# Kernel optimization log

Measured on AMD Instinct MI355X. Metric: run time of the kernel, lower is better.

## Reference

```python
import jax, jax.numpy as jnp
from jax import lax
import numpy as np

B, T, I, H, O = 256, 1024, 64, 25, 64

def setup_inputs() -> dict:
    key = jax.random.key(0)
    ks = jax.random.split(key, 7)
    s_ih = 1.0 / np.sqrt(H)  # PyTorch LSTM init scale (uniform +-1/sqrt(H))
    return {
        "x": jax.random.normal(ks[0], (B, T, I), dtype=jnp.float32),
        "W_ih": jax.random.uniform(ks[1], (4 * H, I), minval=-s_ih, maxval=s_ih, dtype=jnp.float32),
        "W_hh": jax.random.uniform(ks[2], (4 * H, H), minval=-s_ih, maxval=s_ih, dtype=jnp.float32),
        "b_ih": jax.random.uniform(ks[3], (4 * H,), minval=-s_ih, maxval=s_ih, dtype=jnp.float32),
        "b_hh": jax.random.uniform(ks[4], (4 * H,), minval=-s_ih, maxval=s_ih, dtype=jnp.float32),
        "W_fc": jax.random.uniform(ks[5], (O, H), minval=-s_ih, maxval=s_ih, dtype=jnp.float32),
        "b_fc": jax.random.uniform(ks[6], (O,), minval=-s_ih, maxval=s_ih, dtype=jnp.float32),
    }

def reference(x, W_ih, W_hh, b_ih, b_hh, W_fc, b_fc):
    # x: [B, T, I]; PyTorch LSTM gate order: i, f, g, o
    Bh = x.shape[0]
    Hh = W_hh.shape[1]
    # Precompute the input contribution to all gates for all timesteps (one big GEMM).
    gates_x = jnp.einsum('bti,gi->btg', x, W_ih) + b_ih + b_hh  # [B, T, 4H]

    def step(carry, gx):
        h, c = carry
        g = gx + h @ W_hh.T                     # [B, 4H]
        i, f, gg, o = jnp.split(g, 4, axis=-1)
        i = jax.nn.sigmoid(i)
        f = jax.nn.sigmoid(f)
        gg = jnp.tanh(gg)
        o = jax.nn.sigmoid(o)
        c = f * c + i * gg
        h = o * jnp.tanh(c)
        return (h, c), h

    h0 = jnp.zeros((Bh, Hh), dtype=x.dtype)
    c0 = jnp.zeros((Bh, Hh), dtype=x.dtype)
    _, hs = lax.scan(step, (h0, c0), jnp.swapaxes(gates_x, 0, 1))  # hs: [T, B, H]
    hs = jnp.swapaxes(hs, 0, 1)                                   # [B, T, H]
    return hs @ W_fc.T + b_fc                                     # [B, T, O]
```

## Files before the change

### kernel.cpp

```cpp
#include <hip/hip_runtime.h>
#include <hip/hip_fp16.h>


#define Bn 256
#define Tn 1024
#define In 64
#define Hn 25
#define Gn 100
#define On 64
#define CH 16
#define NCH (Tn / CH)

#define SCL_S -1.44269504089f
#define SCL_T -2.88539008178f

typedef __attribute__((ext_vector_type(8))) short short8;
typedef __attribute__((ext_vector_type(4))) float f32x4;
typedef __attribute__((ext_vector_type(4))) int i32x4;

__device__ __forceinline__ float frcp(float x) { return __builtin_amdgcn_rcpf(x); }
__device__ __forceinline__ float ex2(float x) {
    float r;
    asm("v_exp_f32 %0, %1\n\ts_nop 1" : "=v"(r) : "v"(x));
    return r;
}
__device__ __forceinline__ float bcast(float v, int lane) {
    return __int_as_float(__builtin_amdgcn_readlane(__float_as_int(v), lane));
}
__device__ __forceinline__ float xswap(float x) {
    float a = x, b = x;
    asm("s_nop 0\n\tv_permlane32_swap_b32 %0, %1\n\ts_nop 0"
        : "+v"(a), "+v"(b));
    return b;
}
__device__ __forceinline__ unsigned short f2bf(float f) {
    unsigned u = __float_as_uint(f);
    return (unsigned short)((u + 0x7FFFu + ((u >> 16) & 1u)) >> 16);
}
__device__ __forceinline__ int pk2(float lo, float hi) {
    return (int)(((unsigned)f2bf(hi) << 16) | f2bf(lo));
}

__device__ __forceinline__ void colmap(int n, int& g, float& scl) {
    if (n < 50) {
        const int r = n >> 1;
        g = ((n & 1) ? 2 : 0) * Hn + r;
        scl = (n & 1) ? SCL_T : SCL_S;
    } else {
        const int m = n - 50, r = m >> 1;
        g = ((m & 1) ? 3 : 1) * Hn + r;
        scl = SCL_S;
    }
}

__global__ __launch_bounds__(192, 1)
void lstm_fused(const float* __restrict__ x, const float* __restrict__ W_ih,
                const float* __restrict__ W_hh, const float* __restrict__ b_ih,
                const float* __restrict__ b_hh, const float* __restrict__ W_fc,
                const float* __restrict__ b_fc, float* __restrict__ out) {
    __shared__ short lB[112 * 72];
    __shared__ float lbias[112];
    __shared__ short xlds[16 * 72];
    __shared__ float gbuf[2][CH * 100];
    __shared__ float hbuf[32][64];

    const int tid  = threadIdx.x;
    const int wid  = tid >> 6;
    const int lane = tid & 63;
    const int b    = blockIdx.x;

    for (int i = tid; i < 112 * 64; i += 192) {
        const int n = i >> 6, k = i & 63;
        float v = 0.f;
        if (n < Gn) {
            int g; float scl;
            colmap(n, g, scl);
            v = W_ih[(size_t)g * In + k] * scl;
        }
        lB[n * 72 + k] = (short)f2bf(v);
    }
    if (tid < 112) {
        float v = 0.f;
        if (tid < Gn) {
            int g; float scl;
            colmap(tid, g, scl);
            v = (b_ih[g] + b_hh[g]) * scl;
        }
        lbias[tid] = v;
    }
    __syncthreads();

    float wAv[25], wBv[25];
    float c = 0.f, h = 0.f;
    float sB = 1.f, dB = 0.f;
    int coff = 0;
    float wFC[25];
    float bfc = 0.f;
    float* op = nullptr;
    short8 bf0[7], bf1[7];
    float biasv[7];
    float4 xr0, xr1, xr2, xr3;
    const float* xb = x + (size_t)b * Tn * In;

    const int quad = lane >> 4;
    const int l16  = lane & 15;

    if (wid == 0) {
        const bool lo = lane < 32;
        const int rr  = min(lane & 31, Hn - 1);
        const float sclA = SCL_S;
        const float sclB = lo ? SCL_T : SCL_S;
        sB = lo ? 2.f : 1.f;
        dB = lo ? -1.f : 0.f;
        const float* rowA = W_hh + (size_t)((lo ? 0 : 1) * Hn + rr) * Hn;
        const float* rowB = W_hh + (size_t)((lo ? 2 : 3) * Hn + rr) * Hn;
#pragma unroll
        for (int j = 0; j < 25; ++j) {
            wAv[j] = rowA[j] * sclA;
            wBv[j] = rowB[j] * sclB;
        }
        coff = 2 * rr + (lo ? 0 : 50);
    } else if (wid == 1) {
#pragma unroll
        for (int j = 0; j < 25; ++j) wFC[j] = W_fc[(size_t)lane * Hn + j];
        bfc = b_fc[lane];
        op = out + (size_t)b * Tn * On + lane;
    } else {
#pragma unroll
        for (int nt = 0; nt < 7; ++nt) {
            const int col = nt * 16 + l16;
            bf0[nt] = *(const short8*)&lB[col * 72 + 0  + quad * 8];
            bf1[nt] = *(const short8*)&lB[col * 72 + 32 + quad * 8];
            biasv[nt] = lbias[col];
        }
        const int row = lane >> 2, cb = (lane & 3) * 16;
        const float4 a = *(const float4*)(xb + lane * 16 + 0);
        const float4 d = *(const float4*)(xb + lane * 16 + 4);
        const float4 e = *(const float4*)(xb + lane * 16 + 8);
        const float4 f = *(const float4*)(xb + lane * 16 + 12);
        i32x4 p0, p1;
        p0.x = pk2(a.x, a.y); p0.y = pk2(a.z, a.w);
        p0.z = pk2(d.x, d.y); p0.w = pk2(d.z, d.w);
        p1.x = pk2(e.x, e.y); p1.y = pk2(e.z, e.w);
        p1.z = pk2(f.x, f.y); p1.w = pk2(f.z, f.w);
        *(i32x4*)&xlds[row * 72 + cb + 0] = p0;
        *(i32x4*)&xlds[row * 72 + cb + 8] = p1;
    }
    __syncthreads();

    if (wid == 2) {
        const short8 a0 = *(const short8*)&xlds[l16 * 72 + 0  + quad * 8];
        const short8 a1 = *(const short8*)&xlds[l16 * 72 + 32 + quad * 8];
#pragma unroll
        for (int nt = 0; nt < 7; ++nt) {
            f32x4 acc = {biasv[nt], biasv[nt], biasv[nt], biasv[nt]};
            acc = __builtin_amdgcn_mfma_f32_16x16x32_bf16(a0, bf0[nt], acc, 0, 0, 0);
            acc = __builtin_amdgcn_mfma_f32_16x16x32_bf16(a1, bf1[nt], acc, 0, 0, 0);
            const int col = nt * 16 + l16;
            if (col < Gn) {
#pragma unroll
                for (int i = 0; i < 4; ++i)
                    gbuf[0][(quad * 4 + i) * 100 + col] = acc[i];
            }
        }
        const float* xs = xb + 1024;
        xr0 = *(const float4*)(xs + lane * 16 + 0);
        xr1 = *(const float4*)(xs + lane * 16 + 4);
        xr2 = *(const float4*)(xs + lane * 16 + 8);
        xr3 = *(const float4*)(xs + lane * 16 + 12);
    }
    __syncthreads();

#pragma unroll 1
    for (int k = 0; k <= NCH; ++k) {
        if (wid == 0) {
            if (k < NCH) {
                const int kb = k & 1;
                float2 g[CH];
#pragma unroll
                for (int s = 0; s < CH; ++s)
                    g[s] = *(const float2*)&gbuf[kb][s * 100 + coff];
#pragma unroll
                for (int s = 0; s < CH; ++s) {
                    float aA0 = g[s].x, aA1 = 0.f, aA2 = 0.f, aA3 = 0.f;
                    float aB0 = g[s].y, aB1 = 0.f, aB2 = 0.f, aB3 = 0.f;
#pragma unroll
                    for (int j = 0; j < 24; j += 4) {
                        const float h0 = bcast(h, j);
                        const float h1 = bcast(h, j + 1);
                        const float h2 = bcast(h, j + 2);
                        const float h3 = bcast(h, j + 3);
                        aA0 = fmaf(wAv[j],     h0, aA0);
                        aB0 = fmaf(wBv[j],     h0, aB0);
                        aA1 = fmaf(wAv[j + 1], h1, aA1);
                        aB1 = fmaf(wBv[j + 1], h1, aB1);
                        aA2 = fmaf(wAv[j + 2], h2, aA2);
                        aB2 = fmaf(wBv[j + 2], h2, aB2);
                        aA3 = fmaf(wAv[j + 3], h3, aA3);
                        aB3 = fmaf(wBv[j + 3], h3, aB3);
                    }
                    {
                        const float h0 = bcast(h, 24);
                        aA0 = fmaf(wAv[24], h0, aA0);
                        aB0 = fmaf(wBv[24], h0, aB0);
                    }
                    const float aA = (aA0 + aA1) + (aA2 + aA3);
                    const float aB = (aB0 + aB1) + (aB2 + aB3);

                    const float rA = frcp(1.f + ex2(aA));
                    const float rB = frcp(1.f + ex2(aB));
                    const float Fg = xswap(rA);
                    const float Og = xswap(rB);
                    const float actB = fmaf(sB, rB, dB);
                    c = fmaf(Fg, c, rA * actB);
                    const float r2 = frcp(1.f + ex2(c * SCL_T));
                    h = fmaf(Og + Og, r2, -Og);

                    hbuf[(k * CH + s) & 31][lane] = h;
                }
            }
        } else if (wid == 1) {
            if (k >= 1) {
#pragma unroll
                for (int s = 0; s < CH; ++s) {
                    const int t = (k - 1) * CH + s;
                    const int sl = t & 31;
                    float a0 = bfc, a1 = 0.f;
#pragma unroll
                    for (int j = 0; j < 24; j += 2) {
                        a0 = fmaf(hbuf[sl][j],     wFC[j],     a0);
                        a1 = fmaf(hbuf[sl][j + 1], wFC[j + 1], a1);
                    }
                    a0 = fmaf(hbuf[sl][24], wFC[24], a0);
                    op[(size_t)t * On] = a0 + a1;
                }
            }
        } else {
            if (k < NCH - 1) {
                const int row = lane >> 2, cb = (lane & 3) * 16;
                i32x4 p0, p1;
                p0.x = pk2(xr0.x, xr0.y); p0.y = pk2(xr0.z, xr0.w);
                p0.z = pk2(xr1.x, xr1.y); p0.w = pk2(xr1.z, xr1.w);
                p1.x = pk2(xr2.x, xr2.y); p1.y = pk2(xr2.z, xr2.w);
                p1.z = pk2(xr3.x, xr3.y); p1.w = pk2(xr3.z, xr3.w);
                *(i32x4*)&xlds[row * 72 + cb + 0] = p0;
                *(i32x4*)&xlds[row * 72 + cb + 8] = p1;
                if (k < NCH - 2) {
                    const float* xs = xb + (size_t)(k + 2) * (CH * In);
                    xr0 = *(const float4*)(xs + lane * 16 + 0);
                    xr1 = *(const float4*)(xs + lane * 16 + 4);
                    xr2 = *(const float4*)(xs + lane * 16 + 8);
                    xr3 = *(const float4*)(xs + lane * 16 + 12);
                }
                asm volatile("s_waitcnt lgkmcnt(0)" ::: "memory");
                const short8 a0 = *(const short8*)&xlds[l16 * 72 + 0  + quad * 8];
                const short8 a1 = *(const short8*)&xlds[l16 * 72 + 32 + quad * 8];
                const int nb = (k + 1) & 1;
#pragma unroll
                for (int nt = 0; nt < 7; ++nt) {
                    f32x4 acc = {biasv[nt], biasv[nt], biasv[nt], biasv[nt]};
                    acc = __builtin_amdgcn_mfma_f32_16x16x32_bf16(a0, bf0[nt], acc, 0, 0, 0);
                    acc = __builtin_amdgcn_mfma_f32_16x16x32_bf16(a1, bf1[nt], acc, 0, 0, 0);
                    const int col = nt * 16 + l16;
                    if (col < Gn) {
#pragma unroll
                        for (int i = 0; i < 4; ++i)
                            gbuf[nb][(quad * 4 + i) * 100 + col] = acc[i];
                    }
                }
            }
        }
        asm volatile("s_waitcnt lgkmcnt(0)" ::: "memory");
        __builtin_amdgcn_s_barrier();
        asm volatile("" ::: "memory");
    }
}

extern "C" void kernel_launch(void* const* d_in, const int* in_sizes, int n_in,
                              void* d_out, int out_size, void* d_ws, size_t ws_size,
                              hipStream_t stream) {
    const float* x    = (const float*)d_in[0];
    const float* W_ih = (const float*)d_in[1];
    const float* W_hh = (const float*)d_in[2];
    const float* b_ih = (const float*)d_in[3];
    const float* b_hh = (const float*)d_in[4];
    const float* W_fc = (const float*)d_in[5];
    const float* b_fc = (const float*)d_in[6];
    float* out = (float*)d_out;

    lstm_fused<<<Bn, 192, 0, stream>>>(x, W_ih, W_hh, b_ih, b_hh,
                                       W_fc, b_fc, out);
}
```

Baseline: 319.2 us.

## Process two batch elements per block with interleaved recurrence chains

Each block now handles two batch elements, and the grid is halved. The recurrence wave interleaves two independent LSTM chains to expose instruction-level parallelism, which hides the readlane and transcendental latency. The MFMA tile's 16 rows are split as 8 timesteps for each of the two sequences, which halves the chunk size. The trade-off is twice the serial work per wave and only half the CUs occupied.

Result: slower. 490.8 us (+53.8%).

```diff
diff --git a/kernel.cpp b/kernel.cpp
--- a/kernel.cpp
+++ b/kernel.cpp
@@ -8,7 +8,7 @@
 #define Hn 25
 #define Gn 100
 #define On 64
-#define CH 16
+#define CH 8
 #define NCH (Tn / CH)
 
 #define SCL_S -1.44269504089f
@@ -54,20 +54,21 @@
 }
 
 __global__ __launch_bounds__(192, 1)
-void lstm_fused(const float* __restrict__ x, const float* __restrict__ W_ih,
-                const float* __restrict__ W_hh, const float* __restrict__ b_ih,
-                const float* __restrict__ b_hh, const float* __restrict__ W_fc,
-                const float* __restrict__ b_fc, float* __restrict__ out) {
+void lstm_fused2(const float* __restrict__ x, const float* __restrict__ W_ih,
+                 const float* __restrict__ W_hh, const float* __restrict__ b_ih,
+                 const float* __restrict__ b_hh, const float* __restrict__ W_fc,
+                 const float* __restrict__ b_fc, float* __restrict__ out) {
     __shared__ short lB[112 * 72];
     __shared__ float lbias[112];
     __shared__ short xlds[16 * 72];
-    __shared__ float gbuf[2][CH * 100];
-    __shared__ float hbuf[32][64];
+    __shared__ float gbuf[2][2][CH * 100];
+    __shared__ float hbuf[2][16][64];
 
     const int tid  = threadIdx.x;
     const int wid  = tid >> 6;
     const int lane = tid & 63;
-    const int b    = blockIdx.x;
+    const int blk  = blockIdx.x;
+    const int bA   = 2 * blk;
 
     for (int i = tid; i < 112 * 64; i += 192) {
         const int n = i >> 6, k = i & 63;
@@ -91,19 +92,23 @@
     __syncthreads();
 
     float wAv[25], wBv[25];
-    float c = 0.f, h = 0.f;
+    float cA = 0.f, hA = 0.f;
+    float cB = 0.f, hB = 0.f;
     float sB = 1.f, dB = 0.f;
     int coff = 0;
     float wFC[25];
     float bfc = 0.f;
-    float* op = nullptr;
+    float *opA = nullptr, *opB = nullptr;
     short8 bf0[7], bf1[7];
     float biasv[7];
     float4 xr0, xr1, xr2, xr3;
-    const float* xb = x + (size_t)b * Tn * In;
 
     const int quad = lane >> 4;
     const int l16  = lane & 15;
+    const int xrow  = lane >> 2;
+    const int xc4   = (lane & 3) * 16;
+    const float* xsrc0 = x + (size_t)(bA + (xrow >> 3)) * Tn * In
+                           + (size_t)(xrow & 7) * In + xc4;
 
     if (wid == 0) {
         const bool lo = lane < 32;
@@ -124,7 +129,8 @@
 #pragma unroll
         for (int j = 0; j < 25; ++j) wFC[j] = W_fc[(size_t)lane * Hn + j];
         bfc = b_fc[lane];
-        op = out + (size_t)b * Tn * On + lane;
+        opA = out + (size_t)bA * Tn * On + lane;
+        opB = out + (size_t)(bA + 1) * Tn * On + lane;
     } else {
 #pragma unroll
         for (int nt = 0; nt < 7; ++nt) {
@@ -133,24 +139,24 @@
             bf1[nt] = *(const short8*)&lB[col * 72 + 32 + quad * 8];
             biasv[nt] = lbias[col];
         }
-        const int row = lane >> 2, cb = (lane & 3) * 16;
-        const float4 a = *(const float4*)(xb + lane * 16 + 0);
-        const float4 d = *(const float4*)(xb + lane * 16 + 4);
-        const float4 e = *(const float4*)(xb + lane * 16 + 8);
-        const float4 f = *(const float4*)(xb + lane * 16 + 12);
+        const float4 a = *(const float4*)(xsrc0 + 0);
+        const float4 d = *(const float4*)(xsrc0 + 4);
+        const float4 e = *(const float4*)(xsrc0 + 8);
+        const float4 f = *(const float4*)(xsrc0 + 12);
         i32x4 p0, p1;
         p0.x = pk2(a.x, a.y); p0.y = pk2(a.z, a.w);
         p0.z = pk2(d.x, d.y); p0.w = pk2(d.z, d.w);
         p1.x = pk2(e.x, e.y); p1.y = pk2(e.z, e.w);
         p1.z = pk2(f.x, f.y); p1.w = pk2(f.z, f.w);
-        *(i32x4*)&xlds[row * 72 + cb + 0] = p0;
-        *(i32x4*)&xlds[row * 72 + cb + 8] = p1;
+        *(i32x4*)&xlds[xrow * 72 + xc4 + 0] = p0;
+        *(i32x4*)&xlds[xrow * 72 + xc4 + 8] = p1;
     }
     __syncthreads();
 
     if (wid == 2) {
         const short8 a0 = *(const short8*)&xlds[l16 * 72 + 0  + quad * 8];
         const short8 a1 = *(const short8*)&xlds[l16 * 72 + 32 + quad * 8];
+        const int obat = quad >> 1, os = (quad & 1) * 4;
 #pragma unroll
         for (int nt = 0; nt < 7; ++nt) {
             f32x4 acc = {biasv[nt], biasv[nt], biasv[nt], biasv[nt]};
@@ -160,14 +166,14 @@
             if (col < Gn) {
 #pragma unroll
                 for (int i = 0; i < 4; ++i)
-                    gbuf[0][(quad * 4 + i) * 100 + col] = acc[i];
+                    gbuf[0][obat][(os + i) * 100 + col] = acc[i];
             }
         }
-        const float* xs = xb + 1024;
-        xr0 = *(const float4*)(xs + lane * 16 + 0);
-        xr1 = *(const float4*)(xs + lane * 16 + 4);
-        xr2 = *(const float4*)(xs + lane * 16 + 8);
-        xr3 = *(const float4*)(xs + lane * 16 + 12);
+        const float* xs = xsrc0 + CH * In;
+        xr0 = *(const float4*)(xs + 0);
+        xr1 = *(const float4*)(xs + 4);
+        xr2 = *(const float4*)(xs + 8);
+        xr3 = *(const float4*)(xs + 12);
     }
     __syncthreads();
 
@@ -176,47 +182,62 @@
         if (wid == 0) {
             if (k < NCH) {
                 const int kb = k & 1;
-                float2 g[CH];
-#pragma unroll
-                for (int s = 0; s < CH; ++s)
-                    g[s] = *(const float2*)&gbuf[kb][s * 100 + coff];
+                float2 gA[CH], gB[CH];
 #pragma unroll
                 for (int s = 0; s < CH; ++s) {
-                    float aA0 = g[s].x, aA1 = 0.f, aA2 = 0.f, aA3 = 0.f;
-                    float aB0 = g[s].y, aB1 = 0.f, aB2 = 0.f, aB3 = 0.f;
-#pragma unroll
-                    for (int j = 0; j < 24; j += 4) {
-                        const float h0 = bcast(h, j);
-                        const float h1 = bcast(h, j + 1);
-                        const float h2 = bcast(h, j + 2);
-                        const float h3 = bcast(h, j + 3);
-                        aA0 = fmaf(wAv[j],     h0, aA0);
-                        aB0 = fmaf(wBv[j],     h0, aB0);
-                        aA1 = fmaf(wAv[j + 1], h1, aA1);
-                        aB1 = fmaf(wBv[j + 1], h1, aB1);
-                        aA2 = fmaf(wAv[j + 2], h2, aA2);
-                        aB2 = fmaf(wBv[j + 2], h2, aB2);
-                        aA3 = fmaf(wAv[j + 3], h3, aA3);
-                        aB3 = fmaf(wBv[j + 3], h3, aB3);
+                    gA[s] = *(const float2*)&gbuf[kb][0][s * 100 + coff];
+                    gB[s] = *(const float2*)&gbuf[kb][1][s * 100 + coff];
+                }
+#pragma unroll
+                for (int s = 0; s < CH; ++s) {
+                    float pA0 = gA[s].x, pA1 = 0.f;
+                    float qA0 = gA[s].y, qA1 = 0.f;
+                    float pB0 = gB[s].x, pB1 = 0.f;
+                    float qB0 = gB[s].y, qB1 = 0.f;
+#pragma unroll
+                    for (int j = 0; j < 24; j += 2) {
+                        const float a0 = bcast(hA, j);
+                        const float a1 = bcast(hA, j + 1);
+                        const float b0 = bcast(hB, j);
+                        const float b1 = bcast(hB, j + 1);
+                        pA0 = fmaf(wAv[j],     a0, pA0);
+                        qA0 = fmaf(wBv[j],     a0, qA0);
+                        pB0 = fmaf(wAv[j],     b0, pB0);
+                        qB0 = fmaf(wBv[j],     b0, qB0);
+                        pA1 = fmaf(wAv[j + 1], a1, pA1);
+                        qA1 = fmaf(wBv[j + 1], a1, qA1);
+                        pB1 = fmaf(wAv[j + 1], b1, pB1);
+                        qB1 = fmaf(wBv[j + 1], b1, qB1);
                     }
                     {
-                        const float h0 = bcast(h, 24);
-                        aA0 = fmaf(wAv[24], h0, aA0);
-                        aB0 = fmaf(wBv[24], h0, aB0);
+                        const float a0 = bcast(hA, 24);
+                        const float b0 = bcast(hB, 24);
+                        pA0 = fmaf(wAv[24], a0, pA0);
+                        qA0 = fmaf(wBv[24], a0, qA0);
+                        pB0 = fmaf(wAv[24], b0, pB0);
+                        qB0 = fmaf(wBv[24], b0, qB0);
                     }
-                    const float aA = (aA0 + aA1) + (aA2 + aA3);
-                    const float aB = (aB0 + aB1) + (aB2 + aB3);
-
-                    const float rA = frcp(1.f + ex2(aA));
-                    const float rB = frcp(1.f + ex2(aB));
-                    const float Fg = xswap(rA);
-                    const float Og = xswap(rB);
-                    const float actB = fmaf(sB, rB, dB);
-                    c = fmaf(Fg, c, rA * actB);
-                    const float r2 = frcp(1.f + ex2(c * SCL_T));
-                    h = fmaf(Og + Og, r2, -Og);
-
-                    hbuf[(k * CH + s) & 31][lane] = h;
+                    const float aAA = pA0 + pA1, aBA = qA0 + qA1;
+                    const float aAB = pB0 + pB1, aBB = qB0 + qB1;
+
+                    const float rAA = frcp(1.f + ex2(aAA));
+                    const float rBA = frcp(1.f + ex2(aBA));
+                    const float rAB = frcp(1.f + ex2(aAB));
+                    const float rBB = frcp(1.f + ex2(aBB));
+                    const float FgA = xswap(rAA), OgA = xswap(rBA);
+                    const float FgB = xswap(rAB), OgB = xswap(rBB);
+                    const float acA = fmaf(sB, rBA, dB);
+                    const float acB = fmaf(sB, rBB, dB);
+                    cA = fmaf(FgA, cA, rAA * acA);
+                    cB = fmaf(FgB, cB, rAB * acB);
+                    const float r2A = frcp(1.f + ex2(cA * SCL_T));
+                    const float r2B = frcp(1.f + ex2(cB * SCL_T));
+                    hA = fmaf(OgA + OgA, r2A, -OgA);
+                    hB = fmaf(OgB + OgB, r2B, -OgB);
+
+                    const int sl = (k * CH + s) & 15;
+                    hbuf[0][sl][lane] = hA;
+                    hbuf[1][sl][lane] = hB;
                 }
             }
         } else if (wid == 1) {
@@ -224,38 +245,42 @@
 #pragma unroll
                 for (int s = 0; s < CH; ++s) {
                     const int t = (k - 1) * CH + s;
-                    const int sl = t & 31;
-                    float a0 = bfc, a1 = 0.f;
+                    const int sl = t & 15;
+                    float a0 = bfc, a1 = 0.f, b0 = bfc, b1 = 0.f;
 #pragma unroll
                     for (int j = 0; j < 24; j += 2) {
-                        a0 = fmaf(hbuf[sl][j],     wFC[j],     a0);
-                        a1 = fmaf(hbuf[sl][j + 1], wFC[j + 1], a1);
+                        a0 = fmaf(hbuf[0][sl][j],     wFC[j],     a0);
+                        a1 = fmaf(hbuf[0][sl][j + 1], wFC[j + 1], a1);
+                        b0 = fmaf(hbuf[1][sl][j],     wFC[j],     b0);
+                        b1 = fmaf(hbuf[1][sl][j + 1], wFC[j + 1], b1);
                     }
-                    a0 = fmaf(hbuf[sl][24], wFC[24], a0);
-                    op[(size_t)t * On] = a0 + a1;
+                    a0 = fmaf(hbuf[0][sl][24], wFC[24], a0);
+                    b0 = fmaf(hbuf[1][sl][24], wFC[24], b0);
+                    opA[(size_t)t * On] = a0 + a1;
+                    opB[(size_t)t * On] = b0 + b1;
                 }
             }
         } else {
             if (k < NCH - 1) {
-                const int row = lane >> 2, cb = (lane & 3) * 16;
                 i32x4 p0, p1;
                 p0.x = pk2(xr0.x, xr0.y); p0.y = pk2(xr0.z, xr0.w);
                 p0.z = pk2(xr1.x, xr1.y); p0.w = pk2(xr1.z, xr1.w);
                 p1.x = pk2(xr2.x, xr2.y); p1.y = pk2(xr2.z, xr2.w);
                 p1.z = pk2(xr3.x, xr3.y); p1.w = pk2(xr3.z, xr3.w);
-                *(i32x4*)&xlds[row * 72 + cb + 0] = p0;
-                *(i32x4*)&xlds[row * 72 + cb + 8] = p1;
+                *(i32x4*)&xlds[xrow * 72 + xc4 + 0] = p0;
+                *(i32x4*)&xlds[xrow * 72 + xc4 + 8] = p1;
                 if (k < NCH - 2) {
-                    const float* xs = xb + (size_t)(k + 2) * (CH * In);
-                    xr0 = *(const float4*)(xs + lane * 16 + 0);
-                    xr1 = *(const float4*)(xs + lane * 16 + 4);
-                    xr2 = *(const float4*)(xs + lane * 16 + 8);
-                    xr3 = *(const float4*)(xs + lane * 16 + 12);
+                    const float* xs = xsrc0 + (size_t)(k + 2) * (CH * In);
+                    xr0 = *(const float4*)(xs + 0);
+                    xr1 = *(const float4*)(xs + 4);
+                    xr2 = *(const float4*)(xs + 8);
+                    xr3 = *(const float4*)(xs + 12);
                 }
                 asm volatile("s_waitcnt lgkmcnt(0)" ::: "memory");
                 const short8 a0 = *(const short8*)&xlds[l16 * 72 + 0  + quad * 8];
                 const short8 a1 = *(const short8*)&xlds[l16 * 72 + 32 + quad * 8];
                 const int nb = (k + 1) & 1;
+                const int obat = quad >> 1, os = (quad & 1) * 4;
 #pragma unroll
                 for (int nt = 0; nt < 7; ++nt) {
                     f32x4 acc = {biasv[nt], biasv[nt], biasv[nt], biasv[nt]};
@@ -265,7 +290,7 @@
                     if (col < Gn) {
 #pragma unroll
                         for (int i = 0; i < 4; ++i)
-                            gbuf[nb][(quad * 4 + i) * 100 + col] = acc[i];
+                            gbuf[nb][obat][(os + i) * 100 + col] = acc[i];
                     }
                 }
             }
@@ -288,6 +313,6 @@
     const float* b_fc = (const float*)d_in[6];
     float* out = (float*)d_out;
 
-    lstm_fused<<<Bn, 192, 0, stream>>>(x, W_ih, W_hh, b_ih, b_hh,
-                                       W_fc, b_fc, out);
-}
+    lstm_fused2<<<Bn / 2, 192, 0, stream>>>(x, W_ih, W_hh, b_ih, b_hh,
+                                            W_fc, b_fc, out);
+}
```
